# Optimization experiments

Measured on AMD Instinct MI355X. Metric: run time of the kernel, lower is better.

Reference implementation:

```python
import math
import jax, jax.numpy as jnp
import numpy as np

N_HEADS = 16
D_EMBED = 1024
D_HEAD = D_EMBED // N_HEADS


def setup_inputs() -> dict:
    key = jax.random.key(0)
    k1, k2, k3, k4, k5 = jax.random.split(key, 5)
    B, S, D = 4, 2048, D_EMBED
    scale = 1.0 / math.sqrt(D)
    return {
        "x": jax.random.normal(k1, (B, S, D), dtype=jnp.float32),
        "in_proj_w": jax.random.normal(k2, (3 * D, D), dtype=jnp.float32) * scale,
        "in_proj_b": jax.random.normal(k3, (3 * D,), dtype=jnp.float32) * 0.02,
        "out_proj_w": jax.random.normal(k4, (D, D), dtype=jnp.float32) * scale,
        "out_proj_b": jax.random.normal(k5, (D,), dtype=jnp.float32) * 0.02,
        "causal_mask": 0,
    }


def reference(x, in_proj_w, in_proj_b, out_proj_w, out_proj_b, causal_mask):
    B, S, D = x.shape
    # in_proj: torch Linear -> x @ W^T + b, then chunk into q,k,v
    qkv = x @ in_proj_w.T + in_proj_b              # [B,S,3D]
    q, k, v = jnp.split(qkv, 3, axis=-1)
    # [B,S,D] -> [B,H,S,d]
    def heads(t):
        return t.reshape(B, S, N_HEADS, D_HEAD).transpose(0, 2, 1, 3)
    q, k, v = heads(q), heads(k), heads(v)
    weight = jnp.einsum("bhsd,bhtd->bhst", q, k)   # [B,H,S,S] materialized scores
    if causal_mask:
        mask = jnp.triu(jnp.ones((S, S), dtype=bool), k=1)
        weight = jnp.where(mask, -jnp.inf, weight)
    weight = jax.nn.softmax(weight / math.sqrt(D_HEAD), axis=-1)
    out = jnp.einsum("bhst,bhtd->bhsd", weight, v)  # [B,H,S,d]
    out = out.transpose(0, 2, 1, 3).reshape(B, S, D)
    return out @ out_proj_w.T + out_proj_b
```

## Files before the change

kernel.cpp:

```cpp
#include <hip/hip_runtime.h>

typedef unsigned short u16;
typedef _Float16 h8 __attribute__((ext_vector_type(8)));
typedef __fp16 fp16x2 __attribute__((ext_vector_type(2)));
typedef float f32x4 __attribute__((ext_vector_type(4)));

constexpr int B_ = 4, S_ = 2048, D_ = 1024, H_ = 16;

__device__ __forceinline__ void async16(const void* g, void* l) {
  __builtin_amdgcn_global_load_lds(
      (const __attribute__((address_space(1))) void*)g,
      (__attribute__((address_space(3))) void*)l, 16, 0, 0);
}

__device__ __forceinline__ unsigned pk2(float a, float b) {
  union { fp16x2 h; unsigned u; } c;
  c.h = __builtin_amdgcn_cvt_pkrtz(a, b);
  return c.u;
}

__global__ __launch_bounds__(256) void cvt_kernel(
    const float* __restrict__ src, _Float16* __restrict__ dst, int n)
{
  const int i = (blockIdx.x * 256 + threadIdx.x) * 4;
  if (i >= n) return;
  const float4 v = *(const float4*)(src + i);
  uint2 o;
  o.x = pk2(v.x, v.y);
  o.y = pk2(v.z, v.w);
  *(uint2*)(dst + i) = o;
}

template<bool OUT_HALF>
__global__ __launch_bounds__(256, 2) void gemm_wide(
    const _Float16* __restrict__ A, const _Float16* __restrict__ Bw,
    const float* __restrict__ bias, void* __restrict__ Cout,
    int M, int N, int K)
{
  __shared__ __align__(16) _Float16 sA[2][4096];
  __shared__ __align__(16) _Float16 sB[2][8192];

  const int tid = threadIdx.x;
  const int lane = tid & 63, w = tid >> 6;
  const int wm = w & 1, wn = w >> 1;
  const int m0 = blockIdx.y * 128, n0 = blockIdx.x * 256;

  const int sr = 16 * w + (lane & 15);
  const int ss = lane >> 4;
  const _Float16* gA1 = A + (size_t)(m0 + sr) * K + 8 * ss;
  const _Float16* gA2 = gA1 + (size_t)64 * K;
  const _Float16* gB1 = Bw + (size_t)(n0 + sr) * K + 8 * ss;

  const f32x4 zf = {0.f, 0.f, 0.f, 0.f};
  f32x4 acc[4][8];
#pragma unroll
  for (int i = 0; i < 4; ++i)
#pragma unroll
    for (int j = 0; j < 8; ++j) acc[i][j] = zf;

  async16(gA1, &sA[0][w * 512]);
  async16(gA2, &sA[0][(w + 4) * 512]);
#pragma unroll
  for (int t = 0; t < 4; ++t)
    async16(gB1 + (size_t)(64 * t) * K, &sB[0][(w + 4 * t) * 512]);

  const int NIT = K >> 5;
  for (int it = 0; it < NIT; ++it) {
    const int cur = it & 1;
    __syncthreads();
    if (it + 1 < NIT) {
      const int kn = (it + 1) << 5;
      async16(gA1 + kn, &sA[cur ^ 1][w * 512]);
      async16(gA2 + kn, &sA[cur ^ 1][(w + 4) * 512]);
#pragma unroll
      for (int t = 0; t < 4; ++t)
        async16(gB1 + (size_t)(64 * t) * K + kn, &sB[cur ^ 1][(w + 4 * t) * 512]);
    }

    h8 fa[4], fb[8];
#pragma unroll
    for (int i = 0; i < 4; ++i)
      fa[i] = *(const h8*)&sA[cur][((wm * 4 + i) << 9) + (lane << 3)];
#pragma unroll
    for (int j = 0; j < 8; ++j)
      fb[j] = *(const h8*)&sB[cur][((wn * 8 + j) << 9) + (lane << 3)];
#pragma unroll
    for (int i = 0; i < 4; ++i)
#pragma unroll
      for (int j = 0; j < 8; ++j)
        acc[i][j] = __builtin_amdgcn_mfma_f32_16x16x32_f16(fa[i], fb[j], acc[i][j], 0, 0, 0);
  }

  const int g = lane >> 4, cc = lane & 15;
#pragma unroll
  for (int j = 0; j < 8; ++j) {
    const int col = n0 + (wn * 8 + j) * 16 + cc;
    const float bv = bias[col];
#pragma unroll
    for (int i = 0; i < 4; ++i) {
      const int rowb = m0 + (wm * 4 + i) * 16 + g * 4;
#pragma unroll
      for (int r = 0; r < 4; ++r) {
        const float v = acc[i][j][r] + bv;
        if constexpr (OUT_HALF)
          ((_Float16*)Cout)[(size_t)(rowb + r) * N + col] = (_Float16)v;
        else
          ((float*)Cout)[(size_t)(rowb + r) * N + col] = v;
      }
    }
  }
}

template<bool OUT_HALF>
__global__ __launch_bounds__(256) void gemm_f16(
    const _Float16* __restrict__ A, const _Float16* __restrict__ Bw,
    const float* __restrict__ bias, void* __restrict__ Cout,
    int M, int N, int K)
{
  __shared__ __align__(16) _Float16 sA[2][4096];
  __shared__ __align__(16) _Float16 sB[2][4096];

  const int tid = threadIdx.x;
  const int lane = tid & 63, w = tid >> 6;
  const int wm = w & 1, wn = w >> 1;
  const int m0 = blockIdx.y * 128, n0 = blockIdx.x * 128;

  const int sr = 16 * w + (lane & 15);
  const int ss = lane >> 4;
  const _Float16* gA1 = A + (size_t)(m0 + sr) * K + 8 * ss;
  const _Float16* gA2 = gA1 + (size_t)64 * K;
  const _Float16* gB1 = Bw + (size_t)(n0 + sr) * K + 8 * ss;
  const _Float16* gB2 = gB1 + (size_t)64 * K;

  const f32x4 zf = {0.f, 0.f, 0.f, 0.f};
  f32x4 acc[4][4];
#pragma unroll
  for (int i = 0; i < 4; ++i)
#pragma unroll
    for (int j = 0; j < 4; ++j) acc[i][j] = zf;

  async16(gA1, &sA[0][w * 512]);
  async16(gA2, &sA[0][(w + 4) * 512]);
  async16(gB1, &sB[0][w * 512]);
  async16(gB2, &sB[0][(w + 4) * 512]);

  const int NIT = K >> 5;
  for (int it = 0; it < NIT; ++it) {
    const int cur = it & 1;
    __syncthreads();
    if (it + 1 < NIT) {
      const int kn = (it + 1) << 5;
      async16(gA1 + kn, &sA[cur ^ 1][w * 512]);
      async16(gA2 + kn, &sA[cur ^ 1][(w + 4) * 512]);
      async16(gB1 + kn, &sB[cur ^ 1][w * 512]);
      async16(gB2 + kn, &sB[cur ^ 1][(w + 4) * 512]);
    }

    h8 fa[4], fb[4];
#pragma unroll
    for (int i = 0; i < 4; ++i) {
      fa[i] = *(const h8*)&sA[cur][((wm * 4 + i) << 9) + (lane << 3)];
      fb[i] = *(const h8*)&sB[cur][((wn * 4 + i) << 9) + (lane << 3)];
    }
#pragma unroll
    for (int i = 0; i < 4; ++i)
#pragma unroll
      for (int j = 0; j < 4; ++j)
        acc[i][j] = __builtin_amdgcn_mfma_f32_16x16x32_f16(fa[i], fb[j], acc[i][j], 0, 0, 0);
  }

  const int g = lane >> 4, cc = lane & 15;
#pragma unroll
  for (int j = 0; j < 4; ++j) {
    const int col = n0 + (wn * 4 + j) * 16 + cc;
    const float bv = bias[col];
#pragma unroll
    for (int i = 0; i < 4; ++i) {
      const int rowb = m0 + (wm * 4 + i) * 16 + g * 4;
#pragma unroll
      for (int r = 0; r < 4; ++r) {
        const float v = acc[i][j][r] + bv;
        if constexpr (OUT_HALF)
          ((_Float16*)Cout)[(size_t)(rowb + r) * N + col] = (_Float16)v;
        else
          ((float*)Cout)[(size_t)(rowb + r) * N + col] = v;
      }
    }
  }
}

__global__ __launch_bounds__(256) void transpose_v(
    const u16* __restrict__ qkv, u16* __restrict__ vT)
{
  __shared__ u16 T[64 * 73];
  const int tid = threadIdx.x;
  const int bh = blockIdx.y, s0 = blockIdx.x * 64;
  const int b = bh >> 4, h = bh & 15;
#pragma unroll
  for (int t = 0; t < 2; ++t) {
    const int c = tid + t * 256, r = c >> 3, cs = c & 7;
    union { int4 v; u16 s[8]; } u;
    u.v = *(const int4*)(qkv + (size_t)(b * S_ + s0 + r) * 3072 + 2048 + h * 64 + 8 * cs);
#pragma unroll
    for (int i = 0; i < 8; ++i) T[r * 73 + 8 * cs + i] = u.s[i];
  }
  __syncthreads();
#pragma unroll
  for (int t = 0; t < 2; ++t) {
    const int c = tid + t * 256, rd = c >> 3, ss = c & 7;
    union { int4 v; u16 s[8]; } u;
#pragma unroll
    for (int i = 0; i < 8; ++i) u.s[i] = T[(8 * ss + i) * 73 + rd];
    *(int4*)(vT + (size_t)(bh * 64 + rd) * S_ + s0 + 8 * ss) = u.v;
  }
}

__global__ __launch_bounds__(256, 4) void attn_f16(
    const _Float16* __restrict__ qkv, const _Float16* __restrict__ vT,
    _Float16* __restrict__ attnO, const int* __restrict__ causal_ptr)
{
  __shared__ __align__(16) _Float16 sQP[9216];
  __shared__ __align__(16) _Float16 sK[4096];
  __shared__ __align__(16) _Float16 sV[4096];

  const int tid = threadIdx.x, lane = tid & 63, w = tid >> 6;
  const int q4 = lane >> 4, cc = lane & 15;
  const int bh = blockIdx.y, b = bh >> 4, h = bh & 15;
  const int q0 = blockIdx.x * 128;
  const int causal = causal_ptr[0];

  {
    const int rr = lane & 15, sc8 = lane >> 4;
#pragma unroll
    for (int tt = 0; tt < 2; ++tt) {
      const int t = 2 * w + tt;
#pragma unroll
      for (int sh = 0; sh < 2; ++sh) {
        const _Float16* g = qkv + (size_t)(b * S_ + q0 + 16 * t + rr) * 3072 + h * 64 + 8 * (4 * sh + sc8);
        async16(g, &sQP[t * 1024 + sh * 512]);
      }
    }
  }
  __syncthreads();

  h8 qf[2][2];
#pragma unroll
  for (int m = 0; m < 2; ++m)
#pragma unroll
    for (int kk = 0; kk < 2; ++kk) {
      h8 v = *(const h8*)&sQP[((2 * w + m) << 10) + (kk << 9) + (lane << 3)];
      qf[m][kk] = v * (_Float16)0.18033688f;
    }

  h8 ones;
#pragma unroll
  for (int i = 0; i < 8; ++i) ones[i] = (_Float16)1.0f;

  const _Float16* gK = qkv + (size_t)(b * S_ + 16 * w + (lane & 15)) * 3072 + 1024 + h * 64 + 8 * (lane >> 4);
  const _Float16* gV = vT + (size_t)(bh * 64 + 16 * w + (lane & 15)) * S_ + 8 * (lane >> 4);
  _Float16* lK0 = &sK[w * 1024];
  _Float16* lV0 = &sV[w * 1024];

  const int wp = w * 2304;

  const f32x4 zf = {0.f, 0.f, 0.f, 0.f};
  f32x4 oa[2][4], lac[2];
#pragma unroll
  for (int m = 0; m < 2; ++m) {
    lac[m] = zf;
#pragma unroll
    for (int nt = 0; nt < 4; ++nt) oa[m][nt] = zf;
  }

  const int nit = causal ? (q0 / 64 + 2) : (S_ / 64);

  for (int it = 0; it < nit; ++it) {
    const int j0 = it * 64;
    __syncthreads();
    async16(gK + (size_t)j0 * 3072, lK0);
    async16(gK + (size_t)j0 * 3072 + 32, lK0 + 512);
    async16(gV + j0, lV0);
    async16(gV + j0 + 32, lV0 + 512);
    __syncthreads();

    f32x4 sc[2][4];
#pragma unroll
    for (int nt = 0; nt < 4; ++nt) {
      const h8 kf0 = *(const h8*)&sK[(nt << 10) + (lane << 3)];
      const h8 kf1 = *(const h8*)&sK[(nt << 10) + 512 + (lane << 3)];
#pragma unroll
      for (int m = 0; m < 2; ++m) {
        sc[m][nt] = __builtin_amdgcn_mfma_f32_16x16x32_f16(kf0, qf[m][0], zf, 0, 0, 0);
        sc[m][nt] = __builtin_amdgcn_mfma_f32_16x16x32_f16(kf1, qf[m][1], sc[m][nt], 0, 0, 0);
      }
    }

    if (causal) {
#pragma unroll
      for (int m = 0; m < 2; ++m)
#pragma unroll
        for (int nt = 0; nt < 4; ++nt)
#pragma unroll
          for (int r = 0; r < 4; ++r)
            if ((j0 + nt * 16 + q4 * 4 + r) > (q0 + 32 * w + m * 16 + cc))
              sc[m][nt][r] = -1.0e30f;
    }

#pragma unroll
    for (int m = 0; m < 2; ++m)
#pragma unroll
      for (int nt = 0; nt < 4; ++nt) {
        uint2 pk;
        pk.x = pk2(exp2f(sc[m][nt][0]), exp2f(sc[m][nt][1]));
        pk.y = pk2(exp2f(sc[m][nt][2]), exp2f(sc[m][nt][3]));
        *(uint2*)&sQP[wp + (m * 16 + cc) * 72 + nt * 16 + q4 * 4] = pk;
      }

    asm volatile("s_waitcnt lgkmcnt(0)" ::: "memory");

    h8 pf[2][2];
#pragma unroll
    for (int m = 0; m < 2; ++m)
#pragma unroll
      for (int kk = 0; kk < 2; ++kk)
        pf[m][kk] = *(const h8*)&sQP[wp + (m * 16 + cc) * 72 + kk * 32 + q4 * 8];

#pragma unroll
    for (int m = 0; m < 2; ++m) {
      lac[m] = __builtin_amdgcn_mfma_f32_16x16x32_f16(pf[m][0], ones, lac[m], 0, 0, 0);
      lac[m] = __builtin_amdgcn_mfma_f32_16x16x32_f16(pf[m][1], ones, lac[m], 0, 0, 0);
    }
#pragma unroll
    for (int nt = 0; nt < 4; ++nt) {
      const h8 vf0 = *(const h8*)&sV[(nt << 10) + (lane << 3)];
      const h8 vf1 = *(const h8*)&sV[(nt << 10) + 512 + (lane << 3)];
#pragma unroll
      for (int m = 0; m < 2; ++m) {
        oa[m][nt] = __builtin_amdgcn_mfma_f32_16x16x32_f16(pf[m][0], vf0, oa[m][nt], 0, 0, 0);
        oa[m][nt] = __builtin_amdgcn_mfma_f32_16x16x32_f16(pf[m][1], vf1, oa[m][nt], 0, 0, 0);
      }
    }
  }

#pragma unroll
  for (int m = 0; m < 2; ++m) {
    float inv[4];
#pragma unroll
    for (int r = 0; r < 4; ++r) inv[r] = 1.0f / lac[m][r];
#pragma unroll
    for (int nt = 0; nt < 4; ++nt) {
      const int col = h * 64 + nt * 16 + cc;
#pragma unroll
      for (int r = 0; r < 4; ++r) {
        const int row = b * S_ + q0 + 32 * w + m * 16 + q4 * 4 + r;
        attnO[(size_t)row * D_ + col] = (_Float16)(oa[m][nt][r] * inv[r]);
      }
    }
  }
}

extern "C" void kernel_launch(void* const* d_in, const int* in_sizes, int n_in,
                              void* d_out, int out_size, void* d_ws, size_t ws_size,
                              hipStream_t stream)
{
  const float* x  = (const float*)d_in[0];
  const float* wi = (const float*)d_in[1];
  const float* bi = (const float*)d_in[2];
  const float* wo = (const float*)d_in[3];
  const float* bo = (const float*)d_in[4];
  const int* causal = (const int*)d_in[5];

  _Float16* xh   = (_Float16*)d_ws;
  _Float16* wih  = xh + 8388608;
  _Float16* woh  = wih + 3145728;
  _Float16* qkvb = woh + 1048576;
  _Float16* vT   = qkvb + 25165824;
  _Float16* attn = vT + 8388608;

  const int M = B_ * S_;

  cvt_kernel<<<8192, 256, 0, stream>>>(x, xh, M * D_);
  cvt_kernel<<<3072, 256, 0, stream>>>(wi, wih, 3 * D_ * D_);
  cvt_kernel<<<1024, 256, 0, stream>>>(wo, woh, D_ * D_);

  gemm_wide<true><<<dim3(12, 64), 256, 0, stream>>>(
      xh, wih, bi, qkvb, M, 3 * D_, D_);

  transpose_v<<<dim3(32, 64), 256, 0, stream>>>((const u16*)qkvb, (u16*)vT);

  attn_f16<<<dim3(16, 64), 256, 0, stream>>>(qkvb, vT, attn, causal);

  gemm_f16<false><<<dim3(8, 64), 256, 0, stream>>>(
      attn, woh, bo, d_out, M, D_, D_);
}
```

Measured before the change: 351.3 us.

## Use two waves per attention block, each handling 64 query rows

The attention kernel now runs 128 threads (2 waves) per block instead of 4 waves, and each wave processes 64 query rows (4 m-tiles) instead of 32. Each K/V fragment loaded from LDS is reused across twice as many MFMAs, and each wave issues more of the K/V tile loads. Score computation is restructured per nt so only 4 score accumulators are live at once. The cost is higher register pressure, since output accumulators double, and fewer waves per block to hide latency. The block-level sync count per tile stays the same.

```diff
diff --git a/kernel.cpp b/kernel.cpp
--- a/kernel.cpp
+++ b/kernel.cpp
@@ -215,7 +215,7 @@
   }
 }
 
-__global__ __launch_bounds__(256, 4) void attn_f16(
+__global__ __launch_bounds__(128, 2) void attn_f16(
     const _Float16* __restrict__ qkv, const _Float16* __restrict__ vT,
     _Float16* __restrict__ attnO, const int* __restrict__ causal_ptr)
 {
@@ -229,26 +229,25 @@
   const int q0 = blockIdx.x * 128;
   const int causal = causal_ptr[0];
 
-  {
-    const int rr = lane & 15, sc8 = lane >> 4;
-#pragma unroll
-    for (int tt = 0; tt < 2; ++tt) {
-      const int t = 2 * w + tt;
-#pragma unroll
-      for (int sh = 0; sh < 2; ++sh) {
-        const _Float16* g = qkv + (size_t)(b * S_ + q0 + 16 * t + rr) * 3072 + h * 64 + 8 * (4 * sh + sc8);
-        async16(g, &sQP[t * 1024 + sh * 512]);
-      }
+  const int rr = lane & 15, sc8 = lane >> 4;
+
+#pragma unroll
+  for (int tt = 0; tt < 4; ++tt) {
+    const int t = 4 * w + tt;
+#pragma unroll
+    for (int sh = 0; sh < 2; ++sh) {
+      const _Float16* g = qkv + (size_t)(b * S_ + q0 + 16 * t + rr) * 3072 + h * 64 + 8 * (4 * sh + sc8);
+      async16(g, &sQP[t * 1024 + sh * 512]);
     }
   }
   __syncthreads();
 
-  h8 qf[2][2];
-#pragma unroll
-  for (int m = 0; m < 2; ++m)
+  h8 qf[4][2];
+#pragma unroll
+  for (int m = 0; m < 4; ++m)
 #pragma unroll
     for (int kk = 0; kk < 2; ++kk) {
-      h8 v = *(const h8*)&sQP[((2 * w + m) << 10) + (kk << 9) + (lane << 3)];
+      h8 v = *(const h8*)&sQP[((4 * w + m) << 10) + (kk << 9) + (lane << 3)];
       qf[m][kk] = v * (_Float16)0.18033688f;
     }
 
@@ -256,17 +255,12 @@
 #pragma unroll
   for (int i = 0; i < 8; ++i) ones[i] = (_Float16)1.0f;
 
-  const _Float16* gK = qkv + (size_t)(b * S_ + 16 * w + (lane & 15)) * 3072 + 1024 + h * 64 + 8 * (lane >> 4);
-  const _Float16* gV = vT + (size_t)(bh * 64 + 16 * w + (lane & 15)) * S_ + 8 * (lane >> 4);
-  _Float16* lK0 = &sK[w * 1024];
-  _Float16* lV0 = &sV[w * 1024];
-
-  const int wp = w * 2304;
+  const int wp = w * 4608;
 
   const f32x4 zf = {0.f, 0.f, 0.f, 0.f};
-  f32x4 oa[2][4], lac[2];
-#pragma unroll
-  for (int m = 0; m < 2; ++m) {
+  f32x4 oa[4][4], lac[4];
+#pragma unroll
+  for (int m = 0; m < 4; ++m) {
     lac[m] = zf;
 #pragma unroll
     for (int nt = 0; nt < 4; ++nt) oa[m][nt] = zf;
@@ -277,73 +271,74 @@
   for (int it = 0; it < nit; ++it) {
     const int j0 = it * 64;
     __syncthreads();
-    async16(gK + (size_t)j0 * 3072, lK0);
-    async16(gK + (size_t)j0 * 3072 + 32, lK0 + 512);
-    async16(gV + j0, lV0);
-    async16(gV + j0 + 32, lV0 + 512);
+#pragma unroll
+    for (int tt = 0; tt < 2; ++tt) {
+      const int t = 2 * w + tt;
+#pragma unroll
+      for (int sh = 0; sh < 2; ++sh) {
+        const _Float16* gk = qkv + (size_t)(b * S_ + j0 + 16 * t + rr) * 3072 + 1024 + h * 64 + 8 * (4 * sh + sc8);
+        const _Float16* gv = vT + (size_t)(bh * 64 + 16 * t + rr) * S_ + j0 + 8 * (4 * sh + sc8);
+        async16(gk, &sK[t * 1024 + sh * 512]);
+        async16(gv, &sV[t * 1024 + sh * 512]);
+      }
+    }
     __syncthreads();
 
-    f32x4 sc[2][4];
 #pragma unroll
     for (int nt = 0; nt < 4; ++nt) {
       const h8 kf0 = *(const h8*)&sK[(nt << 10) + (lane << 3)];
       const h8 kf1 = *(const h8*)&sK[(nt << 10) + 512 + (lane << 3)];
-#pragma unroll
-      for (int m = 0; m < 2; ++m) {
-        sc[m][nt] = __builtin_amdgcn_mfma_f32_16x16x32_f16(kf0, qf[m][0], zf, 0, 0, 0);
-        sc[m][nt] = __builtin_amdgcn_mfma_f32_16x16x32_f16(kf1, qf[m][1], sc[m][nt], 0, 0, 0);
-      }
-    }
-
-    if (causal) {
-#pragma unroll
-      for (int m = 0; m < 2; ++m)
-#pragma unroll
-        for (int nt = 0; nt < 4; ++nt)
+      f32x4 sc[4];
+#pragma unroll
+      for (int m = 0; m < 4; ++m) {
+        sc[m] = __builtin_amdgcn_mfma_f32_16x16x32_f16(kf0, qf[m][0], zf, 0, 0, 0);
+        sc[m] = __builtin_amdgcn_mfma_f32_16x16x32_f16(kf1, qf[m][1], sc[m], 0, 0, 0);
+      }
+      if (causal) {
+#pragma unroll
+        for (int m = 0; m < 4; ++m)
 #pragma unroll
           for (int r = 0; r < 4; ++r)
-            if ((j0 + nt * 16 + q4 * 4 + r) > (q0 + 32 * w + m * 16 + cc))
-              sc[m][nt][r] = -1.0e30f;
-    }
-
-#pragma unroll
-    for (int m = 0; m < 2; ++m)
-#pragma unroll
-      for (int nt = 0; nt < 4; ++nt) {
+            if ((j0 + nt * 16 + q4 * 4 + r) > (q0 + 64 * w + m * 16 + cc))
+              sc[m][r] = -1.0e30f;
+      }
+#pragma unroll
+      for (int m = 0; m < 4; ++m) {
         uint2 pk;
-        pk.x = pk2(exp2f(sc[m][nt][0]), exp2f(sc[m][nt][1]));
-        pk.y = pk2(exp2f(sc[m][nt][2]), exp2f(sc[m][nt][3]));
+        pk.x = pk2(exp2f(sc[m][0]), exp2f(sc[m][1]));
+        pk.y = pk2(exp2f(sc[m][2]), exp2f(sc[m][3]));
         *(uint2*)&sQP[wp + (m * 16 + cc) * 72 + nt * 16 + q4 * 4] = pk;
       }
+    }
 
     asm volatile("s_waitcnt lgkmcnt(0)" ::: "memory");
 
-    h8 pf[2][2];
-#pragma unroll
-    for (int m = 0; m < 2; ++m)
-#pragma unroll
-      for (int kk = 0; kk < 2; ++kk)
-        pf[m][kk] = *(const h8*)&sQP[wp + (m * 16 + cc) * 72 + kk * 32 + q4 * 8];
-
-#pragma unroll
-    for (int m = 0; m < 2; ++m) {
-      lac[m] = __builtin_amdgcn_mfma_f32_16x16x32_f16(pf[m][0], ones, lac[m], 0, 0, 0);
-      lac[m] = __builtin_amdgcn_mfma_f32_16x16x32_f16(pf[m][1], ones, lac[m], 0, 0, 0);
+    h8 pf0[4], pf1[4];
+#pragma unroll
+    for (int m = 0; m < 4; ++m) {
+      pf0[m] = *(const h8*)&sQP[wp + (m * 16 + cc) * 72 + q4 * 8];
+      pf1[m] = *(const h8*)&sQP[wp + (m * 16 + cc) * 72 + 32 + q4 * 8];
+    }
+
+#pragma unroll
+    for (int m = 0; m < 4; ++m) {
+      lac[m] = __builtin_amdgcn_mfma_f32_16x16x32_f16(pf0[m], ones, lac[m], 0, 0, 0);
+      lac[m] = __builtin_amdgcn_mfma_f32_16x16x32_f16(pf1[m], ones, lac[m], 0, 0, 0);
     }
 #pragma unroll
     for (int nt = 0; nt < 4; ++nt) {
       const h8 vf0 = *(const h8*)&sV[(nt << 10) + (lane << 3)];
       const h8 vf1 = *(const h8*)&sV[(nt << 10) + 512 + (lane << 3)];
 #pragma unroll
-      for (int m = 0; m < 2; ++m) {
-        oa[m][nt] = __builtin_amdgcn_mfma_f32_16x16x32_f16(pf[m][0], vf0, oa[m][nt], 0, 0, 0);
-        oa[m][nt] = __builtin_amdgcn_mfma_f32_16x16x32_f16(pf[m][1], vf1, oa[m][nt], 0, 0, 0);
-      }
-    }
-  }
-
-#pragma unroll
-  for (int m = 0; m < 2; ++m) {
+      for (int m = 0; m < 4; ++m) {
+        oa[m][nt] = __builtin_amdgcn_mfma_f32_16x16x32_f16(pf0[m], vf0, oa[m][nt], 0, 0, 0);
+        oa[m][nt] = __builtin_amdgcn_mfma_f32_16x16x32_f16(pf1[m], vf1, oa[m][nt], 0, 0, 0);
+      }
+    }
+  }
+
+#pragma unroll
+  for (int m = 0; m < 4; ++m) {
     float inv[4];
 #pragma unroll
     for (int r = 0; r < 4; ++r) inv[r] = 1.0f / lac[m][r];
@@ -352,7 +347,7 @@
       const int col = h * 64 + nt * 16 + cc;
 #pragma unroll
       for (int r = 0; r < 4; ++r) {
-        const int row = b * S_ + q0 + 32 * w + m * 16 + q4 * 4 + r;
+        const int row = b * S_ + q0 + 64 * w + m * 16 + q4 * 4 + r;
         attnO[(size_t)row * D_ + col] = (_Float16)(oa[m][nt][r] * inv[r]);
       }
     }
@@ -388,7 +383,7 @@
 
   transpose_v<<<dim3(32, 64), 256, 0, stream>>>((const u16*)qkvb, (u16*)vT);
 
-  attn_f16<<<dim3(16, 64), 256, 0, stream>>>(qkvb, vT, attn, causal);
+  attn_f16<<<dim3(16, 64), 128, 0, stream>>>(qkvb, vT, attn, causal);
 
   gemm_f16<false><<<dim3(8, 64), 256, 0, stream>>>(
       attn, woh, bo, d_out, M, D_, D_);
```

After: 356.0 us. Within noise of the previous version (+1.3%).
